# Kernel tuning notes

Measured on AMD Instinct MI355X. Metric: run time of the kernel, lower is better.

The kernel has to match this reference:

```python
import jax, jax.numpy as jnp
import numpy as np

N, E = 50000, 800000          # nodes, edges (avg degree 16)
D_IN, D_H, D_OUT = 128, 128, 64
BN_EPS = 1e-5


def setup_inputs() -> dict:
    key = jax.random.key(0)
    ks = jax.random.split(key, 8)
    g = lambda k, shp, s: jax.random.normal(k, shp, jnp.float32) * s
    return {
        "x": jax.random.normal(ks[0], (N, D_IN), jnp.float32),
        "edge_index": jax.random.randint(ks[1], (2, E), 0, N),
        # SAGEConv layer 1: lin_l (neighbors, with bias), lin_r (root, no bias)
        "Wl1": g(ks[2], (D_IN, D_H), 0.05),
        "Wr1": g(ks[3], (D_IN, D_H), 0.05),
        "b1": jnp.zeros((D_H,), jnp.float32),
        # BatchNorm1d(hidden)
        "gamma": jnp.ones((D_H,), jnp.float32),
        "beta": jnp.zeros((D_H,), jnp.float32),
        # SAGEConv layer 2
        "Wl2": g(ks[4], (D_H, D_OUT), 0.05),
        "Wr2": g(ks[5], (D_H, D_OUT), 0.05),
        "b2": jnp.zeros((D_OUT,), jnp.float32),
    }


def _sage_conv(x, src, dst, Wl, Wr, b):
    """PyG SAGEConv (mean aggr): lin_l(mean_{j in N(i)} x_j) + lin_r(x_i)."""
    n = x.shape[0]
    agg = jax.ops.segment_sum(x[src], dst, num_segments=n)            # [N, d]
    cnt = jax.ops.segment_sum(jnp.ones((src.shape[0],), x.dtype), dst,
                              num_segments=n)                          # [N]
    agg = agg / jnp.maximum(cnt, 1.0)[:, None]                         # mean, 0 for isolated
    return agg @ Wl + x @ Wr + b


def _batch_norm(x, gamma, beta):
    """Training-mode BatchNorm1d: batch stats over the node axis, biased var."""
    mu = jnp.mean(x, axis=0)
    var = jnp.var(x, axis=0)
    return gamma * (x - mu) * jax.lax.rsqrt(var + BN_EPS) + beta


def reference(x, edge_index, Wl1, Wr1, b1, gamma, beta, Wl2, Wr2, b2):
    src, dst = edge_index[0], edge_index[1]
    h = _sage_conv(x, src, dst, Wl1, Wr1, b1)
    h = jax.nn.relu(_batch_norm(h, gamma, beta))
    # dropout is identity in eval / deterministic reference
    return _sage_conv(h, src, dst, Wl2, Wr2, b2)
```

## Files before the change

kernel.cpp:

```cpp
#include <hip/hip_runtime.h>
#include <hip/hip_bf16.h>
#include <hip/hip_fp8.h>

#define DIN   128
#define DH    128
#define DOUTC 64
#define BN_EPS 1e-5f

typedef __attribute__((ext_vector_type(8))) short bf16x8;
typedef __attribute__((ext_vector_type(4))) float f32x4;
typedef __attribute__((ext_vector_type(2))) float f32x2;

#ifndef __has_builtin
#define __has_builtin(x) 0
#endif
#if __has_builtin(__builtin_amdgcn_cvt_pk_f32_fp8) && __has_builtin(__builtin_amdgcn_cvt_pk_fp8_f32)
#define HW_FP8 1
#else
#define HW_FP8 0
#endif

__device__ inline unsigned short f2bf(float f) {
    __hip_bfloat16 b = __float2bfloat16(f);
    return *reinterpret_cast<unsigned short*>(&b);
}
__device__ inline float bf2f(unsigned short u) {
    return __uint_as_float(((unsigned int)u) << 16);
}
__device__ inline void fp8x4_to_f32(unsigned int w, float* o) {
#if HW_FP8
    f32x2 lo = __builtin_amdgcn_cvt_pk_f32_fp8((int)w, false);
    f32x2 hi = __builtin_amdgcn_cvt_pk_f32_fp8((int)w, true);
    o[0] = lo.x; o[1] = lo.y; o[2] = hi.x; o[3] = hi.y;
#else
    #pragma unroll
    for (int c = 0; c < 4; ++c) {
        __hip_fp8_e4m3 q; q.__x = (__hip_fp8_storage_t)((w >> (8 * c)) & 0xFF);
        o[c] = (float)q;
    }
#endif
}
__device__ inline unsigned int f32x4_to_fp8(float a, float b, float c, float d) {
#if HW_FP8
    int p = __builtin_amdgcn_cvt_pk_fp8_f32(a, b, 0, false);
    p = __builtin_amdgcn_cvt_pk_fp8_f32(c, d, p, true);
    return (unsigned int)p;
#else
    __hip_fp8_e4m3 qa(a), qb(b), qc(c), qd(d);
    return (unsigned int)qa.__x | ((unsigned int)qb.__x << 8) |
           ((unsigned int)qc.__x << 16) | ((unsigned int)qd.__x << 24);
#endif
}

__device__ inline void block_excl_scan_256(const int* __restrict__ arr,
                                           int* __restrict__ excl,
                                           int* __restrict__ wsum, int tid)
{
    int lane = tid & 63, w = tid >> 6;
    int v = arr[tid];
    int inc = v;
    #pragma unroll
    for (int off = 1; off < 64; off <<= 1) {
        int t = __shfl_up(inc, off, 64);
        if (lane >= off) inc += t;
    }
    if (lane == 63) wsum[w] = inc;
    __syncthreads();
    if (tid == 0) {
        int s = 0;
        #pragma unroll
        for (int i = 0; i < 4; ++i) { int t = wsum[i]; wsum[i] = s; s += t; }
    }
    __syncthreads();
    excl[tid] = inc - v + wsum[w];
    __syncthreads();
}

__global__ __launch_bounds__(256) void prep_kernel(
    const float* __restrict__ x, unsigned char* __restrict__ xq,
    const float* __restrict__ Wl1, const float* __restrict__ Wr1,
    const float* __restrict__ Wl2, const float* __restrict__ Wr2,
    unsigned short* __restrict__ W1p, unsigned short* __restrict__ W2p,
    const int* __restrict__ ei, int* __restrict__ cursor,
    unsigned int* __restrict__ coarse,
    int total8, int cvtB, int E, int nb, int cap)
{
    __shared__ int hist[256], lstart[256], gbase[256], wsum[4];
    __shared__ unsigned int staged[4096];
    const int b = blockIdx.x;
    const int tid = threadIdx.x;

    if (b < cvtB) {
        int i = b * 256 + tid;
        if (i >= total8) return;
        float4 a = ((const float4*)x)[2 * i];
        float4 c = ((const float4*)x)[2 * i + 1];
        uint2 pk;
        pk.x = f32x4_to_fp8(a.x, a.y, a.z, a.w);
        pk.y = f32x4_to_fp8(c.x, c.y, c.z, c.w);
        *(uint2*)(xq + (size_t)i * 8) = pk;
        return;
    }
    if (b < cvtB + 192) {
        int region = (b - cvtB) >> 6;
        int idx = ((b - cvtB) & 63) * 256 + tid;
        int k = idx >> 7, c = idx & 127;
        int d = ((k >> 5) * 8 + (c >> 4)) * 512 + ((k >> 3) & 3) * 128 + (c & 15) * 8 + (k & 7);
        if (region == 0)      W1p[d] = f2bf(Wl1[idx]);
        else if (region == 1) W1p[128 * 128 + d] = f2bf(Wr1[idx]);
        else {
            float v = (c < 64) ? Wl2[k * 64 + c] : Wr2[k * 64 + (c - 64)];
            W2p[d] = f2bf(v);
        }
        return;
    }

    const int chunkBase = (b - cvtB - 192) * 4096;
    hist[tid] = 0;
    __syncthreads();

    unsigned int rec[16]; int pos[16]; int bb[16];
    #pragma unroll
    for (int i = 0; i < 16; ++i) {
        int e = chunkBase + i * 256 + tid;
        if (e < E) {
            int s = ei[e], d = ei[E + e];
            rec[i] = ((unsigned int)d << 16) | (unsigned int)s;
            bb[i]  = d >> 8;
            pos[i] = atomicAdd(&hist[bb[i]], 1);
        } else bb[i] = -1;
    }
    __syncthreads();

    block_excl_scan_256(hist, lstart, wsum, tid);

    if (tid < nb) {
        int c = hist[tid];
        gbase[tid] = c ? atomicAdd(&cursor[tid], c) : 0;
    }
    __syncthreads();

    #pragma unroll
    for (int i = 0; i < 16; ++i)
        if (bb[i] >= 0) staged[lstart[bb[i]] + pos[i]] = rec[i];
    __syncthreads();

    int total = min(4096, E - chunkBase);
    for (int i = tid; i < total; i += 256) {
        unsigned int r = staged[i];
        int bk  = (int)(r >> 24);
        int gp  = gbase[bk] + (i - lstart[bk]);
        if (gp < cap) coarse[(size_t)bk * cap + gp] = r;
    }
}

__global__ __launch_bounds__(256) void bin_fine(
    const int* __restrict__ cursor, const unsigned int* __restrict__ coarse,
    unsigned short* __restrict__ sorted, int* __restrict__ deg,
    int* __restrict__ row_start, int n, int cap)
{
    __shared__ int hist[256], pstart[256], cur2[256], wsum[4];
    const int b = blockIdx.x, tid = threadIdx.x;
    const int cnt = min(cursor[b], cap);
    const unsigned int* src = coarse + (size_t)b * cap;

    hist[tid] = 0;
    __syncthreads();

    int nIter = (cnt + 255) >> 8;
    for (int i = 0; i < nIter; ++i) {
        int idx = i * 256 + tid;
        if (idx < cnt) atomicAdd(&hist[(src[idx] >> 16) & 255], 1);
    }
    __syncthreads();

    block_excl_scan_256(hist, pstart, wsum, tid);
    cur2[tid] = pstart[tid];
    __syncthreads();

    for (int i = 0; i < nIter; ++i) {
        int idx = i * 256 + tid;
        if (idx < cnt) {
            unsigned int r = src[idx];
            int dl = (r >> 16) & 255;
            int p  = atomicAdd(&cur2[dl], 1);
            sorted[(size_t)b * cap + p] = (unsigned short)(r & 0xFFFFu);
        }
    }

    int node = b * 256 + tid;
    if (node < n) {
        deg[node]       = hist[tid];
        row_start[node] = b * cap + pstart[tid];
    }
}

__global__ __launch_bounds__(256) void gemm1_fused(
    const unsigned char* __restrict__ xq, const float* __restrict__ x,
    const int* __restrict__ row_start, const int* __restrict__ deg,
    const unsigned short* __restrict__ sorted,
    const unsigned short* __restrict__ W1p, const float* __restrict__ bias,
    unsigned short* __restrict__ hb,
    float* __restrict__ bn_sum, float* __restrict__ bn_sumsq, int n)
{
    __shared__ unsigned short G[64][136];
    __shared__ float red[2][4][128];

    const int block_row = blockIdx.x * 64;
    const int tid  = threadIdx.x;
    const int wave = tid >> 6;
    const int lane = tid & 63;
    const int q    = lane >> 4;
    const int m16  = lane & 15;

    {
        int sub = lane & 7, oct = lane >> 3;
        #pragma unroll
        for (int grp = 0; grp < 2; ++grp) {
            int lr = wave * 16 + grp * 8 + oct;
            int g  = block_row + lr;
            float acc[16];
            #pragma unroll
            for (int j = 0; j < 16; ++j) acc[j] = 0.f;
            int d = 0;
            if (g < n) {
                int base = row_start[g];
                d = deg[g];
                int t = 0;
                for (; t + 8 <= d; t += 8) {
                    uint4 raws[8];
                    #pragma unroll
                    for (int u = 0; u < 8; ++u) {
                        int s = (int)sorted[base + t + u];
                        raws[u] = ((const uint4*)(xq + (size_t)s * DIN))[sub];
                    }
                    #pragma unroll
                    for (int u = 0; u < 8; ++u) {
                        const unsigned int* w = (const unsigned int*)&raws[u];
                        #pragma unroll
                        for (int c = 0; c < 4; ++c) {
                            float o4[4];
                            fp8x4_to_f32(w[c], o4);
                            acc[c*4+0] += o4[0]; acc[c*4+1] += o4[1];
                            acc[c*4+2] += o4[2]; acc[c*4+3] += o4[3];
                        }
                    }
                }
                for (; t < d; ++t) {
                    int s = (int)sorted[base + t];
                    uint4 raw = ((const uint4*)(xq + (size_t)s * DIN))[sub];
                    const unsigned int* w = (const unsigned int*)&raw;
                    #pragma unroll
                    for (int c = 0; c < 4; ++c) {
                        float o4[4];
                        fp8x4_to_f32(w[c], o4);
                        acc[c*4+0] += o4[0]; acc[c*4+1] += o4[1];
                        acc[c*4+2] += o4[2]; acc[c*4+3] += o4[3];
                    }
                }
            }
            float inv = 1.0f / fmaxf((float)d, 1.0f);
            unsigned short t16[16];
            #pragma unroll
            for (int j = 0; j < 16; ++j) t16[j] = f2bf(acc[j] * inv);
            *(uint4*)&G[lr][sub * 16]     = ((uint4*)t16)[0];
            *(uint4*)&G[lr][sub * 16 + 8] = ((uint4*)t16)[1];
        }
    }

    f32x4 acc[8];
    #pragma unroll
    for (int nt = 0; nt < 8; ++nt) acc[nt] = (f32x4){0.f, 0.f, 0.f, 0.f};

    const int grow = block_row + wave * 16 + m16;
    #pragma unroll
    for (int ks = 0; ks < 4; ++ks) {
        bf16x8 ag = *(const bf16x8*)&G[wave * 16 + m16][ks * 32 + q * 8];
        const unsigned short* wp0 = W1p + (size_t)ks * 8 * 512;
        #pragma unroll
        for (int nt = 0; nt < 8; ++nt) {
            bf16x8 b = *(const bf16x8*)(wp0 + nt * 512 + lane * 8);
            acc[nt] = __builtin_amdgcn_mfma_f32_16x16x32_bf16(ag, b, acc[nt], 0, 0, 0);
        }
        bf16x8 ax;
        {
            float4 f0 = {0.f,0.f,0.f,0.f}, f1 = {0.f,0.f,0.f,0.f};
            if (grow < n) {
                const float* xr = x + (size_t)grow * DIN + ks * 32 + q * 8;
                f0 = *(const float4*)xr;
                f1 = *(const float4*)(xr + 4);
            }
            unsigned short t[8];
            t[0]=f2bf(f0.x); t[1]=f2bf(f0.y); t[2]=f2bf(f0.z); t[3]=f2bf(f0.w);
            t[4]=f2bf(f1.x); t[5]=f2bf(f1.y); t[6]=f2bf(f1.z); t[7]=f2bf(f1.w);
            ax = *(bf16x8*)t;
        }
        const unsigned short* wp1 = W1p + (size_t)(4 + ks) * 8 * 512;
        #pragma unroll
        for (int nt = 0; nt < 8; ++nt) {
            bf16x8 b = *(const bf16x8*)(wp1 + nt * 512 + lane * 8);
            acc[nt] = __builtin_amdgcn_mfma_f32_16x16x32_bf16(ax, b, acc[nt], 0, 0, 0);
        }
    }

    float psum[8], psq[8];
    #pragma unroll
    for (int nt = 0; nt < 8; ++nt) {
        int col = nt * 16 + m16;
        float bv = bias[col];
        float s = 0.f, ssq = 0.f;
        #pragma unroll
        for (int reg = 0; reg < 4; ++reg) {
            int g = block_row + wave * 16 + q * 4 + reg;
            float v = acc[nt][reg] + bv;
            if (g < n) {
                hb[(size_t)g * DH + col] = f2bf(v);
                s += v; ssq += v * v;
            }
        }
        psum[nt] = s; psq[nt] = ssq;
    }
    #pragma unroll
    for (int nt = 0; nt < 8; ++nt) {
        psum[nt] += __shfl_xor(psum[nt], 16, 64);
        psum[nt] += __shfl_xor(psum[nt], 32, 64);
        psq[nt]  += __shfl_xor(psq[nt], 16, 64);
        psq[nt]  += __shfl_xor(psq[nt], 32, 64);
    }
    if (lane < 16) {
        #pragma unroll
        for (int nt = 0; nt < 8; ++nt) {
            red[0][wave][nt * 16 + lane] = psum[nt];
            red[1][wave][nt * 16 + lane] = psq[nt];
        }
    }
    __syncthreads();
    if (tid < 128) {
        float s = red[0][0][tid] + red[0][1][tid] + red[0][2][tid] + red[0][3][tid];
        float ssq = red[1][0][tid] + red[1][1][tid] + red[1][2][tid] + red[1][3][tid];
        atomicAdd(&bn_sum[tid], s);
        atomicAdd(&bn_sumsq[tid], ssq);
    }
}

__global__ __launch_bounds__(256) void gemm2p_mfma(
    const unsigned short* __restrict__ hb,
    const float* __restrict__ bn_sum, const float* __restrict__ bn_sumsq,
    const float* __restrict__ gamma, const float* __restrict__ beta,
    const unsigned short* __restrict__ W2p, const float* __restrict__ bias,
    unsigned short* __restrict__ P, float* __restrict__ out, int n)
{
    __shared__ float s_scale[128], s_shift[128];

    const int block_row = blockIdx.x * 64;
    const int tid  = threadIdx.x;
    const int wave = tid >> 6;
    const int lane = tid & 63;
    const int q    = lane >> 4;
    const int m16  = lane & 15;

    if (tid < 128) {
        float invN = 1.0f / (float)n;
        float mu  = bn_sum[tid] * invN;
        float var = bn_sumsq[tid] * invN - mu * mu;
        float sc  = gamma[tid] * rsqrtf(var + BN_EPS);
        s_scale[tid] = sc;
        s_shift[tid] = beta[tid] - mu * sc;
    }
    __syncthreads();

    f32x4 acc[8];
    #pragma unroll
    for (int nt = 0; nt < 8; ++nt) acc[nt] = (f32x4){0.f, 0.f, 0.f, 0.f};

    const int grow = block_row + wave * 16 + m16;
    #pragma unroll
    for (int ks = 0; ks < 4; ++ks) {
        bf16x8 a;
        {
            int kbase = ks * 32 + q * 8;
            float4 sc0 = *(const float4*)&s_scale[kbase];
            float4 sc1 = *(const float4*)&s_scale[kbase + 4];
            float4 sh0 = *(const float4*)&s_shift[kbase];
            float4 sh1 = *(const float4*)&s_shift[kbase + 4];
            unsigned short t[8] = {0,0,0,0,0,0,0,0};
            if (grow < n) {
                uint4 raw = *(const uint4*)(hb + (size_t)grow * DH + kbase);
                const unsigned short* u = (const unsigned short*)&raw;
                t[0] = f2bf(fmaxf(bf2f(u[0]) * sc0.x + sh0.x, 0.f));
                t[1] = f2bf(fmaxf(bf2f(u[1]) * sc0.y + sh0.y, 0.f));
                t[2] = f2bf(fmaxf(bf2f(u[2]) * sc0.z + sh0.z, 0.f));
                t[3] = f2bf(fmaxf(bf2f(u[3]) * sc0.w + sh0.w, 0.f));
                t[4] = f2bf(fmaxf(bf2f(u[4]) * sc1.x + sh1.x, 0.f));
                t[5] = f2bf(fmaxf(bf2f(u[5]) * sc1.y + sh1.y, 0.f));
                t[6] = f2bf(fmaxf(bf2f(u[6]) * sc1.z + sh1.z, 0.f));
                t[7] = f2bf(fmaxf(bf2f(u[7]) * sc1.w + sh1.w, 0.f));
            }
            a = *(bf16x8*)t;
        }
        const unsigned short* wp = W2p + (size_t)ks * 8 * 512;
        #pragma unroll
        for (int nt = 0; nt < 8; ++nt) {
            bf16x8 b = *(const bf16x8*)(wp + nt * 512 + lane * 8);
            acc[nt] = __builtin_amdgcn_mfma_f32_16x16x32_bf16(a, b, acc[nt], 0, 0, 0);
        }
    }

    #pragma unroll
    for (int nt = 0; nt < 4; ++nt) {
        int col = nt * 16 + m16;
        #pragma unroll
        for (int reg = 0; reg < 4; ++reg) {
            int g = block_row + wave * 16 + q * 4 + reg;
            if (g < n) P[(size_t)g * DOUTC + col] = f2bf(acc[nt][reg]);
        }
    }
    #pragma unroll
    for (int nt = 4; nt < 8; ++nt) {
        int col = (nt - 4) * 16 + m16;
        float bv = bias[col];
        #pragma unroll
        for (int reg = 0; reg < 4; ++reg) {
            int g = block_row + wave * 16 + q * 4 + reg;
            if (g < n) out[(size_t)g * DOUTC + col] = acc[nt][reg] + bv;
        }
    }
}

__global__ __launch_bounds__(256) void agg_gather64_add(
    const int* __restrict__ row_start, const int* __restrict__ deg,
    const unsigned short* __restrict__ sorted, const unsigned short* __restrict__ P,
    float* __restrict__ out, int n)
{
    int wid  = (blockIdx.x * 256 + threadIdx.x) >> 6;
    int lane = threadIdx.x & 63;
    int sub = lane & 7, oct = lane >> 3;
    int r = wid * 8 + oct;
    if (r >= n) return;

    float acc[8];
    #pragma unroll
    for (int j = 0; j < 8; ++j) acc[j] = 0.f;

    int base = row_start[r];
    int d    = deg[r];
    int t = 0;
    for (; t + 8 <= d; t += 8) {
        uint4 raws[8];
        #pragma unroll
        for (int u = 0; u < 8; ++u) {
            int s = (int)sorted[base + t + u];
            raws[u] = ((const uint4*)(P + (size_t)s * DOUTC))[sub];
        }
        #pragma unroll
        for (int u = 0; u < 8; ++u) {
            const unsigned short* us = (const unsigned short*)&raws[u];
            #pragma unroll
            for (int j = 0; j < 8; ++j) acc[j] += bf2f(us[j]);
        }
    }
    for (; t < d; ++t) {
        int s = (int)sorted[base + t];
        uint4 raw = ((const uint4*)(P + (size_t)s * DOUTC))[sub];
        const unsigned short* us = (const unsigned short*)&raw;
        #pragma unroll
        for (int j = 0; j < 8; ++j) acc[j] += bf2f(us[j]);
    }
    float inv = 1.0f / fmaxf((float)d, 1.0f);
    float* op = out + (size_t)r * DOUTC + sub * 8;
    float4 c0 = *(float4*)op;
    float4 c1 = *((float4*)op + 1);
    c0.x += acc[0] * inv; c0.y += acc[1] * inv;
    c0.z += acc[2] * inv; c0.w += acc[3] * inv;
    c1.x += acc[4] * inv; c1.y += acc[5] * inv;
    c1.z += acc[6] * inv; c1.w += acc[7] * inv;
    *(float4*)op = c0;
    *((float4*)op + 1) = c1;
}

extern "C" void kernel_launch(void* const* d_in, const int* in_sizes, int n_in,
                              void* d_out, int out_size, void* d_ws, size_t ws_size,
                              hipStream_t stream)
{
    const float* x     = (const float*)d_in[0];
    const int*   ei    = (const int*)  d_in[1];
    const float* Wl1   = (const float*)d_in[2];
    const float* Wr1   = (const float*)d_in[3];
    const float* b1    = (const float*)d_in[4];
    const float* gamma = (const float*)d_in[5];
    const float* beta  = (const float*)d_in[6];
    const float* Wl2   = (const float*)d_in[7];
    const float* Wr2   = (const float*)d_in[8];
    const float* b2    = (const float*)d_in[9];
    float*       out   = (float*)d_out;

    const int N = in_sizes[0] / DIN;
    const int E = in_sizes[1] / 2;

    const int NB  = (N + 255) >> 8;
    int cap = (E / NB) * 3 / 2 + 256;
    cap = (cap + 255) & ~255;

    float* bn_sum   = (float*)d_ws;
    float* bn_sumsq = bn_sum + DH;
    int* cursor     = (int*)(bn_sumsq + DH);
    int* deg        = cursor + 256;
    int* row_start  = deg + N;
    unsigned int* coarse   = (unsigned int*)(row_start + N);
    unsigned short* sorted = (unsigned short*)(coarse + (size_t)NB * cap);
    unsigned short* hb     = sorted + (size_t)NB * cap;
    unsigned short* P      = hb + (size_t)N * DH;
    unsigned short* W1p    = P + (size_t)N * DOUTC;
    unsigned short* W2p    = W1p + 256 * 128;
    unsigned char*  xq     = (unsigned char*)(W2p + 128 * 128);

    hipMemsetAsync(bn_sum, 0, (2 * DH + 256) * sizeof(float), stream);

    dim3 blk(256);
    const int cvtB        = (N * DIN / 8 + 255) / 256;
    const int binA_blocks = (E + 4095) / 4096;
    const int gemm_blocks = (N + 63) / 64;
    const int g64_blocks  = ((N + 7) / 8 + 3) / 4;

    prep_kernel<<<cvtB + 192 + binA_blocks, blk, 0, stream>>>(
        x, xq, Wl1, Wr1, Wl2, Wr2, W1p, W2p,
        ei, cursor, coarse, N * DIN / 8, cvtB, E, NB, cap);

    bin_fine<<<NB, blk, 0, stream>>>(cursor, coarse, sorted, deg, row_start, N, cap);

    gemm1_fused<<<gemm_blocks, blk, 0, stream>>>(xq, x, row_start, deg, sorted,
                                                 W1p, b1, hb, bn_sum, bn_sumsq, N);

    gemm2p_mfma<<<gemm_blocks, blk, 0, stream>>>(hb, bn_sum, bn_sumsq,
                                                 gamma, beta, W2p, b2, P, out, N);

    agg_gather64_add<<<g64_blocks, blk, 0, stream>>>(row_start, deg, sorted,
                                                     P, out, N);
}
```

Baseline: 209.1 us.

## Store P as fp8, split neighbor gather into halves, add nontemporal hints

The intermediate projection P is stored as fp8 instead of bf16, halving the bytes gathered in the second-layer aggregation. The first-layer gather now runs two passes over each neighbor list, each loading only sources in one half of the node range, aiming for better cache locality of the fp8 feature table. Nontemporal loads of x and nontemporal stores of hb are added to reduce cache pollution. The two-pass gather reads each index list twice and adds branches, and fp8 P lowers precision.

```diff
diff --git a/kernel.cpp b/kernel.cpp
--- a/kernel.cpp
+++ b/kernel.cpp
@@ -201,7 +201,7 @@
     const unsigned short* __restrict__ sorted,
     const unsigned short* __restrict__ W1p, const float* __restrict__ bias,
     unsigned short* __restrict__ hb,
-    float* __restrict__ bn_sum, float* __restrict__ bn_sumsq, int n)
+    float* __restrict__ bn_sum, float* __restrict__ bn_sumsq, int n, int H)
 {
     __shared__ unsigned short G[64][136];
     __shared__ float red[2][4][128];
@@ -226,36 +226,44 @@
             if (g < n) {
                 int base = row_start[g];
                 d = deg[g];
-                int t = 0;
-                for (; t + 8 <= d; t += 8) {
-                    uint4 raws[8];
-                    #pragma unroll
-                    for (int u = 0; u < 8; ++u) {
-                        int s = (int)sorted[base + t + u];
-                        raws[u] = ((const uint4*)(xq + (size_t)s * DIN))[sub];
-                    }
-                    #pragma unroll
-                    for (int u = 0; u < 8; ++u) {
-                        const unsigned int* w = (const unsigned int*)&raws[u];
+                for (int half = 0; half < 2; ++half) {
+                    int lo = half ? H : 0;
+                    int hi = half ? n : H;
+                    int t = 0;
+                    for (; t + 8 <= d; t += 8) {
+                        uint4 raws[8];
                         #pragma unroll
-                        for (int c = 0; c < 4; ++c) {
-                            float o4[4];
-                            fp8x4_to_f32(w[c], o4);
-                            acc[c*4+0] += o4[0]; acc[c*4+1] += o4[1];
-                            acc[c*4+2] += o4[2]; acc[c*4+3] += o4[3];
+                        for (int u = 0; u < 8; ++u) {
+                            int s = (int)sorted[base + t + u];
+                            raws[u] = (uint4){0u,0u,0u,0u};
+                            if (s >= lo && s < hi)
+                                raws[u] = ((const uint4*)(xq + (size_t)s * DIN))[sub];
+                        }
+                        #pragma unroll
+                        for (int u = 0; u < 8; ++u) {
+                            const unsigned int* w = (const unsigned int*)&raws[u];
+                            #pragma unroll
+                            for (int c = 0; c < 4; ++c) {
+                                float o4[4];
+                                fp8x4_to_f32(w[c], o4);
+                                acc[c*4+0] += o4[0]; acc[c*4+1] += o4[1];
+                                acc[c*4+2] += o4[2]; acc[c*4+3] += o4[3];
+                            }
                         }
                     }
-                }
-                for (; t < d; ++t) {
-                    int s = (int)sorted[base + t];
-                    uint4 raw = ((const uint4*)(xq + (size_t)s * DIN))[sub];
-                    const unsigned int* w = (const unsigned int*)&raw;
-                    #pragma unroll
-                    for (int c = 0; c < 4; ++c) {
-                        float o4[4];
-                        fp8x4_to_f32(w[c], o4);
-                        acc[c*4+0] += o4[0]; acc[c*4+1] += o4[1];
-                        acc[c*4+2] += o4[2]; acc[c*4+3] += o4[3];
+                    for (; t < d; ++t) {
+                        int s = (int)sorted[base + t];
+                        if (s >= lo && s < hi) {
+                            uint4 raw = ((const uint4*)(xq + (size_t)s * DIN))[sub];
+                            const unsigned int* w = (const unsigned int*)&raw;
+                            #pragma unroll
+                            for (int c = 0; c < 4; ++c) {
+                                float o4[4];
+                                fp8x4_to_f32(w[c], o4);
+                                acc[c*4+0] += o4[0]; acc[c*4+1] += o4[1];
+                                acc[c*4+2] += o4[2]; acc[c*4+3] += o4[3];
+                            }
+                        }
                     }
                 }
             }
@@ -284,11 +292,11 @@
         }
         bf16x8 ax;
         {
-            float4 f0 = {0.f,0.f,0.f,0.f}, f1 = {0.f,0.f,0.f,0.f};
+            f32x4 f0 = {0.f,0.f,0.f,0.f}, f1 = {0.f,0.f,0.f,0.f};
             if (grow < n) {
-                const float* xr = x + (size_t)grow * DIN + ks * 32 + q * 8;
-                f0 = *(const float4*)xr;
-                f1 = *(const float4*)(xr + 4);
+                const f32x4* xr = (const f32x4*)(x + (size_t)grow * DIN + ks * 32 + q * 8);
+                f0 = __builtin_nontemporal_load(xr);
+                f1 = __builtin_nontemporal_load(xr + 1);
             }
             unsigned short t[8];
             t[0]=f2bf(f0.x); t[1]=f2bf(f0.y); t[2]=f2bf(f0.z); t[3]=f2bf(f0.w);
@@ -314,7 +322,7 @@
             int g = block_row + wave * 16 + q * 4 + reg;
             float v = acc[nt][reg] + bv;
             if (g < n) {
-                hb[(size_t)g * DH + col] = f2bf(v);
+                __builtin_nontemporal_store(f2bf(v), hb + (size_t)g * DH + col);
                 s += v; ssq += v * v;
             }
         }
@@ -348,7 +356,7 @@
     const float* __restrict__ bn_sum, const float* __restrict__ bn_sumsq,
     const float* __restrict__ gamma, const float* __restrict__ beta,
     const unsigned short* __restrict__ W2p, const float* __restrict__ bias,
-    unsigned short* __restrict__ P, float* __restrict__ out, int n)
+    unsigned char* __restrict__ P, float* __restrict__ out, int n)
 {
     __shared__ float s_scale[128], s_shift[128];
 
@@ -412,7 +420,10 @@
         #pragma unroll
         for (int reg = 0; reg < 4; ++reg) {
             int g = block_row + wave * 16 + q * 4 + reg;
-            if (g < n) P[(size_t)g * DOUTC + col] = f2bf(acc[nt][reg]);
+            if (g < n) {
+                unsigned int pk = f32x4_to_fp8(acc[nt][reg], 0.f, 0.f, 0.f);
+                P[(size_t)g * DOUTC + col] = (unsigned char)(pk & 0xFF);
+            }
         }
     }
     #pragma unroll
@@ -429,7 +440,7 @@
 
 __global__ __launch_bounds__(256) void agg_gather64_add(
     const int* __restrict__ row_start, const int* __restrict__ deg,
-    const unsigned short* __restrict__ sorted, const unsigned short* __restrict__ P,
+    const unsigned short* __restrict__ sorted, const unsigned char* __restrict__ P,
     float* __restrict__ out, int n)
 {
     int wid  = (blockIdx.x * 256 + threadIdx.x) >> 6;
@@ -446,25 +457,29 @@
     int d    = deg[r];
     int t = 0;
     for (; t + 8 <= d; t += 8) {
-        uint4 raws[8];
+        uint2 raws[8];
         #pragma unroll
         for (int u = 0; u < 8; ++u) {
             int s = (int)sorted[base + t + u];
-            raws[u] = ((const uint4*)(P + (size_t)s * DOUTC))[sub];
+            raws[u] = ((const uint2*)(P + (size_t)s * DOUTC))[sub];
         }
         #pragma unroll
         for (int u = 0; u < 8; ++u) {
-            const unsigned short* us = (const unsigned short*)&raws[u];
-            #pragma unroll
-            for (int j = 0; j < 8; ++j) acc[j] += bf2f(us[j]);
+            float o4[4];
+            fp8x4_to_f32(raws[u].x, o4);
+            acc[0] += o4[0]; acc[1] += o4[1]; acc[2] += o4[2]; acc[3] += o4[3];
+            fp8x4_to_f32(raws[u].y, o4);
+            acc[4] += o4[0]; acc[5] += o4[1]; acc[6] += o4[2]; acc[7] += o4[3];
         }
     }
     for (; t < d; ++t) {
         int s = (int)sorted[base + t];
-        uint4 raw = ((const uint4*)(P + (size_t)s * DOUTC))[sub];
-        const unsigned short* us = (const unsigned short*)&raw;
-        #pragma unroll
-        for (int j = 0; j < 8; ++j) acc[j] += bf2f(us[j]);
+        uint2 raw = ((const uint2*)(P + (size_t)s * DOUTC))[sub];
+        float o4[4];
+        fp8x4_to_f32(raw.x, o4);
+        acc[0] += o4[0]; acc[1] += o4[1]; acc[2] += o4[2]; acc[3] += o4[3];
+        fp8x4_to_f32(raw.y, o4);
+        acc[4] += o4[0]; acc[5] += o4[1]; acc[6] += o4[2]; acc[7] += o4[3];
     }
     float inv = 1.0f / fmaxf((float)d, 1.0f);
     float* op = out + (size_t)r * DOUTC + sub * 8;
@@ -509,10 +524,10 @@
     unsigned int* coarse   = (unsigned int*)(row_start + N);
     unsigned short* sorted = (unsigned short*)(coarse + (size_t)NB * cap);
     unsigned short* hb     = sorted + (size_t)NB * cap;
-    unsigned short* P      = hb + (size_t)N * DH;
-    unsigned short* W1p    = P + (size_t)N * DOUTC;
+    unsigned short* W1p    = hb + (size_t)N * DH;
     unsigned short* W2p    = W1p + 256 * 128;
-    unsigned char*  xq     = (unsigned char*)(W2p + 128 * 128);
+    unsigned char*  P      = (unsigned char*)(W2p + 128 * 128);
+    unsigned char*  xq     = P + (size_t)N * DOUTC;
 
     hipMemsetAsync(bn_sum, 0, (2 * DH + 256) * sizeof(float), stream);
 
@@ -529,7 +544,8 @@
     bin_fine<<<NB, blk, 0, stream>>>(cursor, coarse, sorted, deg, row_start, N, cap);
 
     gemm1_fused<<<gemm_blocks, blk, 0, stream>>>(xq, x, row_start, deg, sorted,
-                                                 W1p, b1, hb, bn_sum, bn_sumsq, N);
+                                                 W1p, b1, hb, bn_sum, bn_sumsq,
+                                                 N, N / 2);
 
     gemm2p_mfma<<<gemm_blocks, blk, 0, stream>>>(hb, bn_sum, bn_sumsq,
                                                  gamma, beta, W2p, b2, P, out, N);
```

Result: slower. 260.4 us (+24.6%).
